# Performance work log

Measured on AMD Instinct MI355X. Metric: run time of the kernel, lower is better.

The kernel has to match this reference:

```python
import jax, jax.numpy as jnp
import numpy as np

HIDDEN = 256


def setup_inputs() -> dict:
    key = jax.random.key(0)
    ks = jax.random.split(key, 6)
    b, c_len, q_len, h = 32, 1024, 128, HIDDEN
    # Xavier-uniform bounds for the learned weights
    lim_vec = float(np.sqrt(6.0 / (h + 1)))      # (h, 1) weights
    lim_cq = float(np.sqrt(6.0 / (1 + h)))       # (1, 1, h) weight
    return {
        "context": jax.random.normal(ks[0], (b, c_len, h), dtype=jnp.float32),
        "query": jax.random.normal(ks[1], (b, q_len, h), dtype=jnp.float32),
        "c_mask": jnp.zeros((b, c_len), dtype=bool),
        "q_mask": jnp.zeros((b, q_len), dtype=bool),
        "c_weight": jax.random.uniform(ks[2], (h, 1), jnp.float32, -lim_vec, lim_vec),
        "q_weight": jax.random.uniform(ks[3], (h, 1), jnp.float32, -lim_vec, lim_vec),
        "cq_weight": jax.random.uniform(ks[4], (1, 1, h), jnp.float32, -lim_cq, lim_cq),
        "bias": jnp.zeros((1,), dtype=jnp.float32),
    }


def reference(context, query, c_mask, q_mask, c_weight, q_weight, cq_weight, bias):
    # Trilinear similarity: S[b,i,j] = c_i.w_c + q_j.w_q + (c_i * w_cq).q_j + bias
    s0 = context @ c_weight                                  # (b, c, 1)
    s1 = jnp.swapaxes(query @ q_weight, 1, 2)                # (b, 1, q)
    s2 = jnp.einsum('bch,bqh->bcq', context * cq_weight, query)
    S = s0 + s1 + s2 + bias                                  # (b, c, q)

    S_bar = jax.nn.softmax(S, axis=1)       # softmax over context axis
    S_bar_bar = jax.nn.softmax(S, axis=2)   # softmax over query axis

    A = jnp.einsum('bcq,bqh->bch', S, query)  # note: raw S, as in source
    B = jnp.einsum('bcq,bkq,bkh->bch', S_bar, S_bar_bar, context)

    return jnp.concatenate([context, A, context * A, context * B], axis=2)
```

## Files before the change

### kernel.cpp

```cpp
#include <hip/hip_runtime.h>
#include <cstdint>
#include <cstddef>

#define BATCH 32
#define CLEN  1024
#define QLEN  128
#define HID   256

typedef __attribute__((ext_vector_type(8))) short bf16x8;
typedef __attribute__((ext_vector_type(4))) float f32x4;

#define MFMA(a, b, c) __builtin_amdgcn_mfma_f32_16x16x32_bf16((a), (b), (c), 0, 0, 0)

__device__ __forceinline__ ushort f2b(float f) {
    union { float f; uint u; } v; v.f = f;
    uint r = (v.u + 0x7fffu + ((v.u >> 16) & 1u)) >> 16;
    return (ushort)r;
}
__device__ __forceinline__ float b2f(ushort u) {
    union { uint u; float f; } v; v.u = ((uint)u) << 16;
    return v.f;
}

__global__ __launch_bounds__(256) void prep_kernel(
    const float* __restrict__ context, const float* __restrict__ query,
    const float* __restrict__ cw, const float* __restrict__ qw,
    const float* __restrict__ cqw,
    ushort* __restrict__ ctxB, ushort* __restrict__ ctxT,
    ushort* __restrict__ qmB, ushort* __restrict__ qT,
    float* __restrict__ cdot, float* __restrict__ qdot)
{
    __shared__ ushort lds[64][258];
    int bid = blockIdx.x;
    int t = threadIdx.x;
    int r = t >> 2, qd = t & 3;
    if (bid < 512) {
        int b = bid >> 4, c0 = (bid & 15) * 64;
        const float* src = context + ((size_t)(b * CLEN + c0 + r)) * HID;
        ushort* cbr = ctxB + ((size_t)(b * CLEN + c0 + r)) * HID;
        float dot = 0.f;
        #pragma unroll
        for (int j = 0; j < 16; j++) {
            int h = j * 16 + qd * 4;
            float4 v = *reinterpret_cast<const float4*>(src + h);
            float4 w = *reinterpret_cast<const float4*>(cw + h);
            dot += v.x * w.x + v.y * w.y + v.z * w.z + v.w * w.w;
            uint p0 = (uint)f2b(v.x) | ((uint)f2b(v.y) << 16);
            uint p1 = (uint)f2b(v.z) | ((uint)f2b(v.w) << 16);
            *reinterpret_cast<uint*>(&lds[r][h])     = p0;
            *reinterpret_cast<uint*>(&lds[r][h + 2]) = p1;
            uint2 pk; pk.x = p0; pk.y = p1;
            *reinterpret_cast<uint2*>(cbr + h) = pk;
        }
        dot += __shfl_xor(dot, 1);
        dot += __shfl_xor(dot, 2);
        if (qd == 0) cdot[b * CLEN + c0 + r] = dot;
        __syncthreads();
        ushort* dst = ctxT + ((size_t)(b * HID + t)) * CLEN + c0;
        #pragma unroll
        for (int j = 0; j < 8; j++) {
            uint4 w;
            w.x = (uint)lds[j*8+0][t] | ((uint)lds[j*8+1][t] << 16);
            w.y = (uint)lds[j*8+2][t] | ((uint)lds[j*8+3][t] << 16);
            w.z = (uint)lds[j*8+4][t] | ((uint)lds[j*8+5][t] << 16);
            w.w = (uint)lds[j*8+6][t] | ((uint)lds[j*8+7][t] << 16);
            *reinterpret_cast<uint4*>(dst + j * 8) = w;
        }
    } else {
        int bb = bid - 512;
        int b = bb >> 1, q0 = (bb & 1) * 64;
        const float* src = query + ((size_t)(b * QLEN + q0 + r)) * HID;
        ushort* qmr = qmB + ((size_t)(b * QLEN + q0 + r)) * HID;
        float dot = 0.f;
        #pragma unroll
        for (int j = 0; j < 16; j++) {
            int h = j * 16 + qd * 4;
            float4 v   = *reinterpret_cast<const float4*>(src + h);
            float4 w   = *reinterpret_cast<const float4*>(qw + h);
            float4 wc4 = *reinterpret_cast<const float4*>(cqw + h);
            dot += v.x * w.x + v.y * w.y + v.z * w.z + v.w * w.w;
            uint p0 = (uint)f2b(v.x) | ((uint)f2b(v.y) << 16);
            uint p1 = (uint)f2b(v.z) | ((uint)f2b(v.w) << 16);
            *reinterpret_cast<uint*>(&lds[r][h])     = p0;
            *reinterpret_cast<uint*>(&lds[r][h + 2]) = p1;
            uint2 mc;
            mc.x = (uint)f2b(v.x * wc4.x) | ((uint)f2b(v.y * wc4.y) << 16);
            mc.y = (uint)f2b(v.z * wc4.z) | ((uint)f2b(v.w * wc4.w) << 16);
            *reinterpret_cast<uint2*>(qmr + h) = mc;
        }
        dot += __shfl_xor(dot, 1);
        dot += __shfl_xor(dot, 2);
        if (qd == 0) qdot[b * QLEN + q0 + r] = dot;
        __syncthreads();
        ushort* dst = qT + ((size_t)(b * HID + t)) * QLEN + q0;
        #pragma unroll
        for (int j = 0; j < 8; j++) {
            uint4 w;
            w.x = (uint)lds[j*8+0][t] | ((uint)lds[j*8+1][t] << 16);
            w.y = (uint)lds[j*8+2][t] | ((uint)lds[j*8+3][t] << 16);
            w.z = (uint)lds[j*8+4][t] | ((uint)lds[j*8+5][t] << 16);
            w.w = (uint)lds[j*8+6][t] | ((uint)lds[j*8+7][t] << 16);
            *reinterpret_cast<uint4*>(dst + j * 8) = w;
        }
    }
}

__global__ __launch_bounds__(256) void s_kernel(
    const ushort* __restrict__ ctxB, const ushort* __restrict__ qmB,
    const float* __restrict__ cdot, const float* __restrict__ qdot,
    const float* __restrict__ bias,
    ushort* __restrict__ S, ushort* __restrict__ P2T)
{
    __shared__ float ldsS[64][132];
    __shared__ float ldsM[64], ldsR[64];
    int ct = blockIdx.x, b = blockIdx.y;
    int c0 = ct * 64;
    int t = threadIdx.x;
    int w = t >> 6, L = t & 63, g = L >> 4, ln = L & 15;
    int wr = w >> 1, wc = w & 1;

    f32x4 acc[2][4];
    #pragma unroll
    for (int mi = 0; mi < 2; mi++)
        #pragma unroll
        for (int ni = 0; ni < 4; ni++) acc[mi][ni] = (f32x4){0.f, 0.f, 0.f, 0.f};

    const ushort* aBase = ctxB + ((size_t)(b * CLEN + c0 + wr * 32)) * HID;
    const ushort* qBb   = qmB + ((size_t)(b * QLEN + wc * 64)) * HID;

    #pragma unroll 2
    for (int kk = 0; kk < 8; kk++) {
        int k = kk * 32 + g * 8;
        bf16x8 a[2], bq[4];
        #pragma unroll
        for (int mi = 0; mi < 2; mi++)
            a[mi] = *reinterpret_cast<const bf16x8*>(aBase + (size_t)(mi * 16 + ln) * HID + k);
        #pragma unroll
        for (int ni = 0; ni < 4; ni++)
            bq[ni] = *reinterpret_cast<const bf16x8*>(qBb + (size_t)(ni * 16 + ln) * HID + k);
        #pragma unroll
        for (int mi = 0; mi < 2; mi++)
            #pragma unroll
            for (int ni = 0; ni < 4; ni++)
                acc[mi][ni] = MFMA(a[mi], bq[ni], acc[mi][ni]);
    }

    float bv = bias[0];
    float qdv[4];
    #pragma unroll
    for (int ni = 0; ni < 4; ni++) qdv[ni] = qdot[b * QLEN + wc * 64 + ni * 16 + ln];
    #pragma unroll
    for (int mi = 0; mi < 2; mi++)
        #pragma unroll
        for (int r = 0; r < 4; r++) {
            int row = wr * 32 + mi * 16 + g * 4 + r;
            float cd = cdot[b * CLEN + c0 + row] + bv;
            #pragma unroll
            for (int ni = 0; ni < 4; ni++)
                ldsS[row][wc * 64 + ni * 16 + ln] = acc[mi][ni][r] + cd + qdv[ni];
        }
    __syncthreads();
    {
        int row = t >> 2, qs = (t & 3) * 32;
        float4 vr[8];
        float m = -1e30f;
        #pragma unroll
        for (int j = 0; j < 8; j++) {
            vr[j] = *reinterpret_cast<const float4*>(&ldsS[row][qs + j * 4]);
            m = fmaxf(m, fmaxf(fmaxf(vr[j].x, vr[j].y), fmaxf(vr[j].z, vr[j].w)));
        }
        m = fmaxf(m, __shfl_xor(m, 1));
        m = fmaxf(m, __shfl_xor(m, 2));
        float s = 0.f;
        #pragma unroll
        for (int j = 0; j < 8; j++)
            s += __expf(vr[j].x - m) + __expf(vr[j].y - m) +
                 __expf(vr[j].z - m) + __expf(vr[j].w - m);
        s += __shfl_xor(s, 1);
        s += __shfl_xor(s, 2);
        if ((t & 3) == 0) { ldsM[row] = m; ldsR[row] = 1.0f / s; }
    }
    __syncthreads();
    {
        const size_t Sbase = ((size_t)b * CLEN + c0) * QLEN;
        #pragma unroll
        for (int i = 0; i < 8; i++) {
            int flat = t + 256 * i;
            int q4 = flat & 31, c = flat >> 5;
            float4 v = *reinterpret_cast<const float4*>(&ldsS[c][q4 * 4]);
            uint2 pk;
            pk.x = (uint)f2b(v.x) | ((uint)f2b(v.y) << 16);
            pk.y = (uint)f2b(v.z) | ((uint)f2b(v.w) << 16);
            *reinterpret_cast<uint2*>(&S[Sbase + (size_t)c * QLEN + q4 * 4]) = pk;
        }
    }
    {
        int q = t >> 1, half = t & 1;
        ushort* dst = P2T + ((size_t)b * QLEN + q) * CLEN + c0 + half * 32;
        #pragma unroll
        for (int jo = 0; jo < 4; jo++) {
            uint pk[4];
            #pragma unroll
            for (int l = 0; l < 4; l++) {
                int c0l = half * 32 + jo * 8 + l * 2;
                float p0 = __expf(ldsS[c0l][q]     - ldsM[c0l])     * ldsR[c0l];
                float p1 = __expf(ldsS[c0l + 1][q] - ldsM[c0l + 1]) * ldsR[c0l + 1];
                pk[l] = (uint)f2b(p0) | ((uint)f2b(p1) << 16);
            }
            uint4 wv; wv.x = pk[0]; wv.y = pk[1]; wv.z = pk[2]; wv.w = pk[3];
            *reinterpret_cast<uint4*>(dst + jo * 8) = wv;
        }
    }
}

__global__ __launch_bounds__(256) void t_kernel(
    const ushort* __restrict__ ctxT, const ushort* __restrict__ P2T,
    float* __restrict__ Tpart)
{
    int x = blockIdx.x, b = blockIdx.y;
    int h0 = (x >> 1) * 64, ks = x & 1;
    int t = threadIdx.x;
    int w = t >> 6, L = t & 63, g = L >> 4, ln = L & 15;
    int wr = w >> 1, wc = w & 1;

    f32x4 acc[2][4];
    #pragma unroll
    for (int mi = 0; mi < 2; mi++)
        #pragma unroll
        for (int ni = 0; ni < 4; ni++) acc[mi][ni] = (f32x4){0.f, 0.f, 0.f, 0.f};

    const ushort* aB = ctxT + ((size_t)(b * HID + h0 + wr * 32)) * CLEN + ks * 512;
    const ushort* bB = P2T + ((size_t)(b * QLEN + wc * 64)) * CLEN + ks * 512;

    #pragma unroll 2
    for (int kk = 0; kk < 16; kk++) {
        int k = kk * 32 + g * 8;
        bf16x8 a[2], bq[4];
        #pragma unroll
        for (int mi = 0; mi < 2; mi++)
            a[mi] = *reinterpret_cast<const bf16x8*>(aB + (size_t)(mi * 16 + ln) * CLEN + k);
        #pragma unroll
        for (int ni = 0; ni < 4; ni++)
            bq[ni] = *reinterpret_cast<const bf16x8*>(bB + (size_t)(ni * 16 + ln) * CLEN + k);
        #pragma unroll
        for (int mi = 0; mi < 2; mi++)
            #pragma unroll
            for (int ni = 0; ni < 4; ni++)
                acc[mi][ni] = MFMA(a[mi], bq[ni], acc[mi][ni]);
    }
    float* dst = Tpart + (size_t)ks * (BATCH * HID * QLEN);
    #pragma unroll
    for (int mi = 0; mi < 2; mi++)
        #pragma unroll
        for (int ni = 0; ni < 4; ni++)
            #pragma unroll
            for (int r = 0; r < 4; r++) {
                int h = h0 + wr * 32 + mi * 16 + g * 4 + r;
                int q = wc * 64 + ni * 16 + ln;
                dst[((size_t)b * HID + h) * QLEN + q] = acc[mi][ni][r];
            }
}

__global__ __launch_bounds__(256) void cs_kernel(
    const ushort* __restrict__ S, const float* __restrict__ Tpart,
    ushort* __restrict__ Tt)
{
    __shared__ float red[4][2][8];
    __shared__ float SR[16];
    int qc = blockIdx.x, b = blockIdx.y;
    int q0 = qc * 16;
    int t = threadIdx.x;
    int qh = t & 1, cg = t >> 1;
    int w = t >> 6, L = t & 63;
    const ushort* base = S + (size_t)b * CLEN * QLEN + q0 + qh * 8;
    float sum[8];
    #pragma unroll
    for (int j = 0; j < 8; j++) sum[j] = 0.f;
    #pragma unroll
    for (int i = 0; i < 8; i++) {
        bf16x8 v = *reinterpret_cast<const bf16x8*>(base + (size_t)(cg + 128 * i) * QLEN);
        #pragma unroll
        for (int j = 0; j < 8; j++) sum[j] += __expf(b2f((ushort)v[j]));
    }
    #pragma unroll
    for (int off = 2; off <= 32; off <<= 1)
        #pragma unroll
        for (int j = 0; j < 8; j++) sum[j] += __shfl_xor(sum[j], off, 64);
    if (L < 2) {
        #pragma unroll
        for (int j = 0; j < 8; j++) red[w][L][j] = sum[j];
    }
    __syncthreads();
    if (t < 16) {
        int j = t & 7, qq = t >> 3;
        float s = red[0][qq][j] + red[1][qq][j] + red[2][qq][j] + red[3][qq][j];
        SR[qq * 8 + j] = 1.0f / s;
    }
    __syncthreads();
    const float* p0 = Tpart + ((size_t)b * HID + t) * QLEN + q0;
    const float* p1 = p0 + (size_t)BATCH * HID * QLEN;
    uint pk[8];
    #pragma unroll
    for (int seg = 0; seg < 4; seg++) {
        float4 xa = *reinterpret_cast<const float4*>(p0 + seg * 4);
        float4 xb = *reinterpret_cast<const float4*>(p1 + seg * 4);
        float r0 = (xa.x + xb.x) * SR[seg * 4 + 0];
        float r1 = (xa.y + xb.y) * SR[seg * 4 + 1];
        float r2 = (xa.z + xb.z) * SR[seg * 4 + 2];
        float r3 = (xa.w + xb.w) * SR[seg * 4 + 3];
        pk[seg * 2 + 0] = (uint)f2b(r0) | ((uint)f2b(r1) << 16);
        pk[seg * 2 + 1] = (uint)f2b(r2) | ((uint)f2b(r3) << 16);
    }
    ushort* dst = Tt + ((size_t)b * HID + t) * QLEN + q0;
    uint4 w0; w0.x = pk[0]; w0.y = pk[1]; w0.z = pk[2]; w0.w = pk[3];
    uint4 w1; w1.x = pk[4]; w1.y = pk[5]; w1.z = pk[6]; w1.w = pk[7];
    *reinterpret_cast<uint4*>(dst)     = w0;
    *reinterpret_cast<uint4*>(dst + 8) = w1;
}

__global__ __launch_bounds__(256) void ab_out_kernel(
    const ushort* __restrict__ S, const ushort* __restrict__ qT,
    const ushort* __restrict__ Tt, const ushort* __restrict__ ctxB,
    float* __restrict__ out)
{
    __shared__ float ldsA[64][68];
    __shared__ float ldsB[64][68];
    int x = blockIdx.x, b = blockIdx.y;
    int c0 = (x >> 1) * 64, h0 = (x & 1) * 128;
    int t = threadIdx.x;
    int wv = t >> 6, L = t & 63, g = L >> 4, ln = L & 15;

    f32x4 accA[4][2], accB[4][2];
    #pragma unroll
    for (int mi = 0; mi < 4; mi++)
        #pragma unroll
        for (int ni = 0; ni < 2; ni++) {
            accA[mi][ni] = (f32x4){0.f, 0.f, 0.f, 0.f};
            accB[mi][ni] = (f32x4){0.f, 0.f, 0.f, 0.f};
        }

    const ushort* Srow = S + ((size_t)(b * CLEN + c0)) * QLEN;
    const ushort* qTb  = qT + ((size_t)(b * HID + h0 + wv * 32)) * QLEN;
    const ushort* TtB  = Tt + ((size_t)(b * HID + h0 + wv * 32)) * QLEN;

    #pragma unroll
    for (int kk = 0; kk < 4; kk++) {
        int k = kk * 32 + g * 8;
        bf16x8 sa[4], pa[4], bq[2], bt[2];
        #pragma unroll
        for (int mi = 0; mi < 4; mi++) {
            sa[mi] = *reinterpret_cast<const bf16x8*>(Srow + (size_t)(mi * 16 + ln) * QLEN + k);
            bf16x8 pv;
            #pragma unroll
            for (int i = 0; i < 8; i++)
                pv[i] = (short)f2b(__expf(b2f((ushort)sa[mi][i])));
            pa[mi] = pv;
        }
        #pragma unroll
        for (int ni = 0; ni < 2; ni++) {
            bq[ni] = *reinterpret_cast<const bf16x8*>(qTb + (size_t)(ni * 16 + ln) * QLEN + k);
            bt[ni] = *reinterpret_cast<const bf16x8*>(TtB + (size_t)(ni * 16 + ln) * QLEN + k);
        }
        #pragma unroll
        for (int mi = 0; mi < 4; mi++)
            #pragma unroll
            for (int ni = 0; ni < 2; ni++) {
                accA[mi][ni] = MFMA(sa[mi], bq[ni], accA[mi][ni]);
                accB[mi][ni] = MFMA(pa[mi], bt[ni], accB[mi][ni]);
            }
    }

    #pragma unroll
    for (int hh = 0; hh < 2; hh++) {
        if ((wv >> 1) == hh) {
            int hc = wv & 1;
            #pragma unroll
            for (int mi = 0; mi < 4; mi++)
                #pragma unroll
                for (int ni = 0; ni < 2; ni++)
                    #pragma unroll
                    for (int r = 0; r < 4; r++) {
                        ldsA[mi * 16 + g * 4 + r][hc * 32 + ni * 16 + ln] = accA[mi][ni][r];
                        ldsB[mi * 16 + g * 4 + r][hc * 32 + ni * 16 + ln] = accB[mi][ni][r];
                    }
        }
        __syncthreads();
        #pragma unroll
        for (int i = 0; i < 2; i++) {
            int flat = t + 256 * i;
            int h8 = flat & 7, c = flat >> 3;
            bf16x8 cb = *reinterpret_cast<const bf16x8*>(
                ctxB + ((size_t)(b * CLEN + c0 + c)) * HID + h0 + hh * 64 + h8 * 8);
            float cf[8];
            #pragma unroll
            for (int j = 0; j < 8; j++) cf[j] = b2f((ushort)cb[j]);
            float4 a0 = *reinterpret_cast<const float4*>(&ldsA[c][h8 * 8]);
            float4 a1 = *reinterpret_cast<const float4*>(&ldsA[c][h8 * 8 + 4]);
            float4 b0 = *reinterpret_cast<const float4*>(&ldsB[c][h8 * 8]);
            float4 b1 = *reinterpret_cast<const float4*>(&ldsB[c][h8 * 8 + 4]);
            size_t o = ((size_t)(b * CLEN + c0 + c)) * 1024 + h0 + hh * 64 + h8 * 8;
            *reinterpret_cast<float4*>(&out[o])     = make_float4(cf[0], cf[1], cf[2], cf[3]);
            *reinterpret_cast<float4*>(&out[o + 4]) = make_float4(cf[4], cf[5], cf[6], cf[7]);
            *reinterpret_cast<float4*>(&out[o + 256]) = a0;
            *reinterpret_cast<float4*>(&out[o + 260]) = a1;
            *reinterpret_cast<float4*>(&out[o + 512]) =
                make_float4(cf[0] * a0.x, cf[1] * a0.y, cf[2] * a0.z, cf[3] * a0.w);
            *reinterpret_cast<float4*>(&out[o + 516]) =
                make_float4(cf[4] * a1.x, cf[5] * a1.y, cf[6] * a1.z, cf[7] * a1.w);
            *reinterpret_cast<float4*>(&out[o + 768]) =
                make_float4(cf[0] * b0.x, cf[1] * b0.y, cf[2] * b0.z, cf[3] * b0.w);
            *reinterpret_cast<float4*>(&out[o + 772]) =
                make_float4(cf[4] * b1.x, cf[5] * b1.y, cf[6] * b1.z, cf[7] * b1.w);
        }
        __syncthreads();
    }
}

extern "C" void kernel_launch(void* const* d_in, const int* in_sizes, int n_in,
                              void* d_out, int out_size, void* d_ws, size_t ws_size,
                              hipStream_t stream)
{
    (void)in_sizes; (void)n_in; (void)out_size; (void)ws_size;
    const float* context   = (const float*)d_in[0];
    const float* query     = (const float*)d_in[1];
    const float* c_weight  = (const float*)d_in[4];
    const float* q_weight  = (const float*)d_in[5];
    const float* cq_weight = (const float*)d_in[6];
    const float* bias      = (const float*)d_in[7];
    float* out = (float*)d_out;
    char* wsb  = (char*)d_ws;

    ushort* ctxB = (ushort*)(wsb);
    ushort* ctxT = (ushort*)(wsb + 16777216);
    ushort* qmB  = (ushort*)(wsb + 33554432);
    ushort* qT   = (ushort*)(wsb + 35651584);
    ushort* S    = (ushort*)(wsb + 37748736);
    ushort* P2T  = (ushort*)(wsb + 46137344);
    ushort* Tt   = (ushort*)(wsb + 54525952);
    float*  Tpart = (float*)(wsb + 56623104);
    float*  cdot  = (float*)(wsb + 65011712);
    float*  qdot  = cdot + 32768;

    prep_kernel<<<576, 256, 0, stream>>>(context, query, c_weight, q_weight,
                                         cq_weight, ctxB, ctxT, qmB, qT,
                                         cdot, qdot);
    s_kernel<<<dim3(16, 32), 256, 0, stream>>>(ctxB, qmB, cdot, qdot, bias, S, P2T);
    t_kernel<<<dim3(8, 32), 256, 0, stream>>>(ctxT, P2T, Tpart);
    cs_kernel<<<dim3(8, 32), 256, 0, stream>>>(S, Tpart, Tt);
    ab_out_kernel<<<dim3(32, 32), 256, 0, stream>>>(S, qT, Tt, ctxB, out);
}
```

Before: 105.9 us.

## Fuse column-softmax sums into S kernel and restructure T and output stages

The S kernel now also emits per-tile column sums of exp(S), so the separate column-sum pass over S in cs_kernel goes away. The reciprocal column sum is applied to P when forming the B operand in ab_out, and cs_kernel becomes a simple elementwise reduce-and-convert kernel. t_kernel's split-K goes from 2 to 4 to launch more blocks, which adds Tpart traffic. Block indices in several kernels are remapped so that blocks sharing a batch run together, likely for L2 locality. The ab_out tile changes to 32 rows by the full hidden width.

Result: slower. 122.9 us (+16.1%).

```diff
diff --git a/kernel.cpp b/kernel.cpp
--- a/kernel.cpp
+++ b/kernel.cpp
@@ -109,11 +109,16 @@
     const ushort* __restrict__ ctxB, const ushort* __restrict__ qmB,
     const float* __restrict__ cdot, const float* __restrict__ qdot,
     const float* __restrict__ bias,
-    ushort* __restrict__ S, ushort* __restrict__ P2T)
+    ushort* __restrict__ S, ushort* __restrict__ P2T,
+    float* __restrict__ psum)
 {
     __shared__ float ldsS[64][132];
     __shared__ float ldsM[64], ldsR[64];
-    int ct = blockIdx.x, b = blockIdx.y;
+    __shared__ float ldsP[2][128];
+    int lin = blockIdx.x + (blockIdx.y << 4);
+    int m = lin >> 3;
+    int b = (lin & 7) | ((m >> 4) << 3);
+    int ct = m & 15;
     int c0 = ct * 64;
     int t = threadIdx.x;
     int w = t >> 6, L = t & 63, g = L >> 4, ln = L & 15;
@@ -163,22 +168,22 @@
     {
         int row = t >> 2, qs = (t & 3) * 32;
         float4 vr[8];
-        float m = -1e30f;
+        float mx = -1e30f;
         #pragma unroll
         for (int j = 0; j < 8; j++) {
             vr[j] = *reinterpret_cast<const float4*>(&ldsS[row][qs + j * 4]);
-            m = fmaxf(m, fmaxf(fmaxf(vr[j].x, vr[j].y), fmaxf(vr[j].z, vr[j].w)));
-        }
-        m = fmaxf(m, __shfl_xor(m, 1));
-        m = fmaxf(m, __shfl_xor(m, 2));
+            mx = fmaxf(mx, fmaxf(fmaxf(vr[j].x, vr[j].y), fmaxf(vr[j].z, vr[j].w)));
+        }
+        mx = fmaxf(mx, __shfl_xor(mx, 1));
+        mx = fmaxf(mx, __shfl_xor(mx, 2));
         float s = 0.f;
         #pragma unroll
         for (int j = 0; j < 8; j++)
-            s += __expf(vr[j].x - m) + __expf(vr[j].y - m) +
-                 __expf(vr[j].z - m) + __expf(vr[j].w - m);
+            s += __expf(vr[j].x - mx) + __expf(vr[j].y - mx) +
+                 __expf(vr[j].z - mx) + __expf(vr[j].w - mx);
         s += __shfl_xor(s, 1);
         s += __shfl_xor(s, 2);
-        if ((t & 3) == 0) { ldsM[row] = m; ldsR[row] = 1.0f / s; }
+        if ((t & 3) == 0) { ldsM[row] = mx; ldsR[row] = 1.0f / s; }
     }
     __syncthreads();
     {
@@ -211,15 +216,37 @@
             *reinterpret_cast<uint4*>(dst + jo * 8) = wv;
         }
     }
+    {
+        int q = t & 127, hf = t >> 7;
+        float s = 0.f;
+        #pragma unroll
+        for (int cc = 0; cc < 32; cc++)
+            s += __expf(b2f(f2b(ldsS[hf * 32 + cc][q])));
+        ldsP[hf][q] = s;
+    }
+    __syncthreads();
+    if (t < 128)
+        psum[((size_t)b * 16 + ct) * QLEN + t] = ldsP[0][t] + ldsP[1][t];
 }
 
 __global__ __launch_bounds__(256) void t_kernel(
     const ushort* __restrict__ ctxT, const ushort* __restrict__ P2T,
-    float* __restrict__ Tpart)
-{
-    int x = blockIdx.x, b = blockIdx.y;
-    int h0 = (x >> 1) * 64, ks = x & 1;
+    const float* __restrict__ psum, float* __restrict__ Tpart,
+    float* __restrict__ colsumr)
+{
+    int lin = blockIdx.x + (blockIdx.y << 4);
+    int m = lin >> 3;
+    int b = (lin & 7) | ((m >> 4) << 3);
+    int x = m & 15;
+    int h0 = (x >> 2) * 64, ks = x & 3;
     int t = threadIdx.x;
+    if (x == 0 && t < QLEN) {
+        float s = 0.f;
+        #pragma unroll
+        for (int j = 0; j < 16; j++)
+            s += psum[((size_t)b * 16 + j) * QLEN + t];
+        colsumr[b * QLEN + t] = 1.0f / s;
+    }
     int w = t >> 6, L = t & 63, g = L >> 4, ln = L & 15;
     int wr = w >> 1, wc = w & 1;
 
@@ -229,11 +256,11 @@
         #pragma unroll
         for (int ni = 0; ni < 4; ni++) acc[mi][ni] = (f32x4){0.f, 0.f, 0.f, 0.f};
 
-    const ushort* aB = ctxT + ((size_t)(b * HID + h0 + wr * 32)) * CLEN + ks * 512;
-    const ushort* bB = P2T + ((size_t)(b * QLEN + wc * 64)) * CLEN + ks * 512;
+    const ushort* aB = ctxT + ((size_t)(b * HID + h0 + wr * 32)) * CLEN + ks * 256;
+    const ushort* bB = P2T + ((size_t)(b * QLEN + wc * 64)) * CLEN + ks * 256;
 
     #pragma unroll 2
-    for (int kk = 0; kk < 16; kk++) {
+    for (int kk = 0; kk < 8; kk++) {
         int k = kk * 32 + g * 8;
         bf16x8 a[2], bq[4];
         #pragma unroll
@@ -261,156 +288,125 @@
             }
 }
 
-__global__ __launch_bounds__(256) void cs_kernel(
-    const ushort* __restrict__ S, const float* __restrict__ Tpart,
-    ushort* __restrict__ Tt)
-{
-    __shared__ float red[4][2][8];
-    __shared__ float SR[16];
-    int qc = blockIdx.x, b = blockIdx.y;
-    int q0 = qc * 16;
-    int t = threadIdx.x;
-    int qh = t & 1, cg = t >> 1;
-    int w = t >> 6, L = t & 63;
-    const ushort* base = S + (size_t)b * CLEN * QLEN + q0 + qh * 8;
-    float sum[8];
-    #pragma unroll
-    for (int j = 0; j < 8; j++) sum[j] = 0.f;
-    #pragma unroll
-    for (int i = 0; i < 8; i++) {
-        bf16x8 v = *reinterpret_cast<const bf16x8*>(base + (size_t)(cg + 128 * i) * QLEN);
-        #pragma unroll
-        for (int j = 0; j < 8; j++) sum[j] += __expf(b2f((ushort)v[j]));
-    }
-    #pragma unroll
-    for (int off = 2; off <= 32; off <<= 1)
-        #pragma unroll
-        for (int j = 0; j < 8; j++) sum[j] += __shfl_xor(sum[j], off, 64);
-    if (L < 2) {
-        #pragma unroll
-        for (int j = 0; j < 8; j++) red[w][L][j] = sum[j];
-    }
-    __syncthreads();
-    if (t < 16) {
-        int j = t & 7, qq = t >> 3;
-        float s = red[0][qq][j] + red[1][qq][j] + red[2][qq][j] + red[3][qq][j];
-        SR[qq * 8 + j] = 1.0f / s;
-    }
-    __syncthreads();
-    const float* p0 = Tpart + ((size_t)b * HID + t) * QLEN + q0;
-    const float* p1 = p0 + (size_t)BATCH * HID * QLEN;
-    uint pk[8];
-    #pragma unroll
-    for (int seg = 0; seg < 4; seg++) {
-        float4 xa = *reinterpret_cast<const float4*>(p0 + seg * 4);
-        float4 xb = *reinterpret_cast<const float4*>(p1 + seg * 4);
-        float r0 = (xa.x + xb.x) * SR[seg * 4 + 0];
-        float r1 = (xa.y + xb.y) * SR[seg * 4 + 1];
-        float r2 = (xa.z + xb.z) * SR[seg * 4 + 2];
-        float r3 = (xa.w + xb.w) * SR[seg * 4 + 3];
-        pk[seg * 2 + 0] = (uint)f2b(r0) | ((uint)f2b(r1) << 16);
-        pk[seg * 2 + 1] = (uint)f2b(r2) | ((uint)f2b(r3) << 16);
-    }
-    ushort* dst = Tt + ((size_t)b * HID + t) * QLEN + q0;
-    uint4 w0; w0.x = pk[0]; w0.y = pk[1]; w0.z = pk[2]; w0.w = pk[3];
-    uint4 w1; w1.x = pk[4]; w1.y = pk[5]; w1.z = pk[6]; w1.w = pk[7];
-    *reinterpret_cast<uint4*>(dst)     = w0;
-    *reinterpret_cast<uint4*>(dst + 8) = w1;
+__global__ __launch_bounds__(256) void tr_kernel(
+    const float* __restrict__ Tpart, ushort* __restrict__ Tt)
+{
+    int gid = blockIdx.x * 256 + threadIdx.x;
+    const float4* p = reinterpret_cast<const float4*>(Tpart);
+    float4 a = p[gid];
+    float4 b = p[gid + 262144];
+    float4 c = p[gid + 524288];
+    float4 d = p[gid + 786432];
+    float4 r = make_float4(a.x + b.x + c.x + d.x, a.y + b.y + c.y + d.y,
+                           a.z + b.z + c.z + d.z, a.w + b.w + c.w + d.w);
+    uint2 pk;
+    pk.x = (uint)f2b(r.x) | ((uint)f2b(r.y) << 16);
+    pk.y = (uint)f2b(r.z) | ((uint)f2b(r.w) << 16);
+    *reinterpret_cast<uint2*>(Tt + (size_t)gid * 4) = pk;
 }
 
 __global__ __launch_bounds__(256) void ab_out_kernel(
     const ushort* __restrict__ S, const ushort* __restrict__ qT,
     const ushort* __restrict__ Tt, const ushort* __restrict__ ctxB,
-    float* __restrict__ out)
-{
-    __shared__ float ldsA[64][68];
-    __shared__ float ldsB[64][68];
-    int x = blockIdx.x, b = blockIdx.y;
-    int c0 = (x >> 1) * 64, h0 = (x & 1) * 128;
+    const float* __restrict__ colsumr, float* __restrict__ out)
+{
+    __shared__ float ldsA[16][260];
+    __shared__ float ldsB[16][260];
+    int lin = blockIdx.x + (blockIdx.y << 5);
+    int m = lin >> 3;
+    int b = (lin & 7) | ((m >> 5) << 3);
+    int ct = m & 31;
+    int c0 = ct * 32;
     int t = threadIdx.x;
     int wv = t >> 6, L = t & 63, g = L >> 4, ln = L & 15;
-
-    f32x4 accA[4][2], accB[4][2];
-    #pragma unroll
-    for (int mi = 0; mi < 4; mi++)
-        #pragma unroll
-        for (int ni = 0; ni < 2; ni++) {
+    int h0w = wv * 64;
+
+    f32x4 accA[2][4], accB[2][4];
+    #pragma unroll
+    for (int mi = 0; mi < 2; mi++)
+        #pragma unroll
+        for (int ni = 0; ni < 4; ni++) {
             accA[mi][ni] = (f32x4){0.f, 0.f, 0.f, 0.f};
             accB[mi][ni] = (f32x4){0.f, 0.f, 0.f, 0.f};
         }
 
     const ushort* Srow = S + ((size_t)(b * CLEN + c0)) * QLEN;
-    const ushort* qTb  = qT + ((size_t)(b * HID + h0 + wv * 32)) * QLEN;
-    const ushort* TtB  = Tt + ((size_t)(b * HID + h0 + wv * 32)) * QLEN;
+    const ushort* qTb  = qT + ((size_t)(b * HID + h0w)) * QLEN;
+    const ushort* TtB  = Tt + ((size_t)(b * HID + h0w)) * QLEN;
+    const float* crB = colsumr + b * QLEN;
 
     #pragma unroll
     for (int kk = 0; kk < 4; kk++) {
         int k = kk * 32 + g * 8;
-        bf16x8 sa[4], pa[4], bq[2], bt[2];
-        #pragma unroll
-        for (int mi = 0; mi < 4; mi++) {
+        float4 cr0 = *reinterpret_cast<const float4*>(crB + k);
+        float4 cr1 = *reinterpret_cast<const float4*>(crB + k + 4);
+        float crv[8] = {cr0.x, cr0.y, cr0.z, cr0.w, cr1.x, cr1.y, cr1.z, cr1.w};
+        bf16x8 sa[2], pa[2], bq[4], bt[4];
+        #pragma unroll
+        for (int mi = 0; mi < 2; mi++) {
             sa[mi] = *reinterpret_cast<const bf16x8*>(Srow + (size_t)(mi * 16 + ln) * QLEN + k);
             bf16x8 pv;
             #pragma unroll
             for (int i = 0; i < 8; i++)
-                pv[i] = (short)f2b(__expf(b2f((ushort)sa[mi][i])));
+                pv[i] = (short)f2b(__expf(b2f((ushort)sa[mi][i])) * crv[i]);
             pa[mi] = pv;
         }
         #pragma unroll
-        for (int ni = 0; ni < 2; ni++) {
+        for (int ni = 0; ni < 4; ni++) {
             bq[ni] = *reinterpret_cast<const bf16x8*>(qTb + (size_t)(ni * 16 + ln) * QLEN + k);
             bt[ni] = *reinterpret_cast<const bf16x8*>(TtB + (size_t)(ni * 16 + ln) * QLEN + k);
         }
         #pragma unroll
-        for (int mi = 0; mi < 4; mi++)
-            #pragma unroll
-            for (int ni = 0; ni < 2; ni++) {
+        for (int mi = 0; mi < 2; mi++)
+            #pragma unroll
+            for (int ni = 0; ni < 4; ni++) {
                 accA[mi][ni] = MFMA(sa[mi], bq[ni], accA[mi][ni]);
                 accB[mi][ni] = MFMA(pa[mi], bt[ni], accB[mi][ni]);
             }
     }
 
     #pragma unroll
-    for (int hh = 0; hh < 2; hh++) {
-        if ((wv >> 1) == hh) {
-            int hc = wv & 1;
-            #pragma unroll
-            for (int mi = 0; mi < 4; mi++)
-                #pragma unroll
-                for (int ni = 0; ni < 2; ni++)
-                    #pragma unroll
-                    for (int r = 0; r < 4; r++) {
-                        ldsA[mi * 16 + g * 4 + r][hc * 32 + ni * 16 + ln] = accA[mi][ni][r];
-                        ldsB[mi * 16 + g * 4 + r][hc * 32 + ni * 16 + ln] = accB[mi][ni][r];
-                    }
-        }
+    for (int ch = 0; ch < 2; ch++) {
+        #pragma unroll
+        for (int ni = 0; ni < 4; ni++)
+            #pragma unroll
+            for (int r = 0; r < 4; r++) {
+                ldsA[g * 4 + r][h0w + ni * 16 + ln] = accA[ch][ni][r];
+                ldsB[g * 4 + r][h0w + ni * 16 + ln] = accB[ch][ni][r];
+            }
         __syncthreads();
-        #pragma unroll
-        for (int i = 0; i < 2; i++) {
-            int flat = t + 256 * i;
-            int h8 = flat & 7, c = flat >> 3;
-            bf16x8 cb = *reinterpret_cast<const bf16x8*>(
-                ctxB + ((size_t)(b * CLEN + c0 + c)) * HID + h0 + hh * 64 + h8 * 8);
-            float cf[8];
-            #pragma unroll
-            for (int j = 0; j < 8; j++) cf[j] = b2f((ushort)cb[j]);
-            float4 a0 = *reinterpret_cast<const float4*>(&ldsA[c][h8 * 8]);
-            float4 a1 = *reinterpret_cast<const float4*>(&ldsA[c][h8 * 8 + 4]);
-            float4 b0 = *reinterpret_cast<const float4*>(&ldsB[c][h8 * 8]);
-            float4 b1 = *reinterpret_cast<const float4*>(&ldsB[c][h8 * 8 + 4]);
-            size_t o = ((size_t)(b * CLEN + c0 + c)) * 1024 + h0 + hh * 64 + h8 * 8;
-            *reinterpret_cast<float4*>(&out[o])     = make_float4(cf[0], cf[1], cf[2], cf[3]);
-            *reinterpret_cast<float4*>(&out[o + 4]) = make_float4(cf[4], cf[5], cf[6], cf[7]);
-            *reinterpret_cast<float4*>(&out[o + 256]) = a0;
-            *reinterpret_cast<float4*>(&out[o + 260]) = a1;
-            *reinterpret_cast<float4*>(&out[o + 512]) =
-                make_float4(cf[0] * a0.x, cf[1] * a0.y, cf[2] * a0.z, cf[3] * a0.w);
-            *reinterpret_cast<float4*>(&out[o + 516]) =
-                make_float4(cf[4] * a1.x, cf[5] * a1.y, cf[6] * a1.z, cf[7] * a1.w);
-            *reinterpret_cast<float4*>(&out[o + 768]) =
-                make_float4(cf[0] * b0.x, cf[1] * b0.y, cf[2] * b0.z, cf[3] * b0.w);
-            *reinterpret_cast<float4*>(&out[o + 772]) =
-                make_float4(cf[4] * b1.x, cf[5] * b1.y, cf[6] * b1.z, cf[7] * b1.w);
+        {
+            int cl = t >> 4, hseg = t & 15;
+            int c = c0 + ch * 16 + cl;
+            const ushort* cbp = ctxB + ((size_t)(b * CLEN + c)) * HID + hseg * 16;
+            bf16x8 cb0 = *reinterpret_cast<const bf16x8*>(cbp);
+            bf16x8 cb1 = *reinterpret_cast<const bf16x8*>(cbp + 8);
+            float cf[16];
+            #pragma unroll
+            for (int j = 0; j < 8; j++) {
+                cf[j]     = b2f((ushort)cb0[j]);
+                cf[j + 8] = b2f((ushort)cb1[j]);
+            }
+            float av[16], bv[16];
+            #pragma unroll
+            for (int j = 0; j < 16; j += 4) {
+                float4 a4 = *reinterpret_cast<const float4*>(&ldsA[cl][hseg * 16 + j]);
+                float4 b4 = *reinterpret_cast<const float4*>(&ldsB[cl][hseg * 16 + j]);
+                av[j] = a4.x; av[j+1] = a4.y; av[j+2] = a4.z; av[j+3] = a4.w;
+                bv[j] = b4.x; bv[j+1] = b4.y; bv[j+2] = b4.z; bv[j+3] = b4.w;
+            }
+            size_t o = ((size_t)(b * CLEN + c)) * 1024 + hseg * 16;
+            #pragma unroll
+            for (int j = 0; j < 16; j += 4) {
+                *reinterpret_cast<float4*>(&out[o + j]) =
+                    make_float4(cf[j], cf[j+1], cf[j+2], cf[j+3]);
+                *reinterpret_cast<float4*>(&out[o + 256 + j]) =
+                    make_float4(av[j], av[j+1], av[j+2], av[j+3]);
+                *reinterpret_cast<float4*>(&out[o + 512 + j]) =
+                    make_float4(cf[j]*av[j], cf[j+1]*av[j+1], cf[j+2]*av[j+2], cf[j+3]*av[j+3]);
+                *reinterpret_cast<float4*>(&out[o + 768 + j]) =
+                    make_float4(cf[j]*bv[j], cf[j+1]*bv[j+1], cf[j+2]*bv[j+2], cf[j+3]*bv[j+3]);
+            }
         }
         __syncthreads();
     }
@@ -438,14 +434,17 @@
     ushort* P2T  = (ushort*)(wsb + 46137344);
     ushort* Tt   = (ushort*)(wsb + 54525952);
     float*  Tpart = (float*)(wsb + 56623104);
-    float*  cdot  = (float*)(wsb + 65011712);
-    float*  qdot  = cdot + 32768;
+    float*  cdot    = (float*)(wsb + 73400320);
+    float*  qdot    = cdot + 32768;
+    float*  colsumr = qdot + 4096;
+    float*  psum    = colsumr + 4096;
 
     prep_kernel<<<576, 256, 0, stream>>>(context, query, c_weight, q_weight,
                                          cq_weight, ctxB, ctxT, qmB, qT,
                                          cdot, qdot);
-    s_kernel<<<dim3(16, 32), 256, 0, stream>>>(ctxB, qmB, cdot, qdot, bias, S, P2T);
-    t_kernel<<<dim3(8, 32), 256, 0, stream>>>(ctxT, P2T, Tpart);
-    cs_kernel<<<dim3(8, 32), 256, 0, stream>>>(S, Tpart, Tt);
-    ab_out_kernel<<<dim3(32, 32), 256, 0, stream>>>(S, qT, Tt, ctxB, out);
-}
+    s_kernel<<<dim3(16, 32), 256, 0, stream>>>(ctxB, qmB, cdot, qdot, bias,
+                                               S, P2T, psum);
+    t_kernel<<<dim3(16, 32), 256, 0, stream>>>(ctxT, P2T, psum, Tpart, colsumr);
+    tr_kernel<<<1024, 256, 0, stream>>>(Tpart, Tt);
+    ab_out_kernel<<<dim3(32, 32), 256, 0, stream>>>(S, qT, Tt, ctxB, colsumr, out);
+}
```

## Fuse column softmax partial sums into S kernel, drop S re-read in cs_kernel

Applied to the files above, without the earlier changes.

The S kernel now computes per-tile column exp-sums (using bf16-rounded S values to match the prior path) and writes them to a small psum buffer. cs_kernel then reduces 16 partials per query instead of re-reading the whole 8 MB bf16 S matrix, and is re-tiled over hidden rows. The ab_out block index mapping also changes so consecutive blocks share h0 and walk c. The cost is extra exp work and one more barrier in the S kernel.

Measured after the change: 99.82 us, median of 2. -5.7%, faster.

```diff
diff --git a/kernel.cpp b/kernel.cpp
--- a/kernel.cpp
+++ b/kernel.cpp
@@ -109,10 +109,12 @@
     const ushort* __restrict__ ctxB, const ushort* __restrict__ qmB,
     const float* __restrict__ cdot, const float* __restrict__ qdot,
     const float* __restrict__ bias,
-    ushort* __restrict__ S, ushort* __restrict__ P2T)
+    ushort* __restrict__ S, ushort* __restrict__ P2T,
+    float* __restrict__ psum)
 {
     __shared__ float ldsS[64][132];
     __shared__ float ldsM[64], ldsR[64];
+    __shared__ float ldsP[2][128];
     int ct = blockIdx.x, b = blockIdx.y;
     int c0 = ct * 64;
     int t = threadIdx.x;
@@ -163,22 +165,22 @@
     {
         int row = t >> 2, qs = (t & 3) * 32;
         float4 vr[8];
-        float m = -1e30f;
+        float mx = -1e30f;
         #pragma unroll
         for (int j = 0; j < 8; j++) {
             vr[j] = *reinterpret_cast<const float4*>(&ldsS[row][qs + j * 4]);
-            m = fmaxf(m, fmaxf(fmaxf(vr[j].x, vr[j].y), fmaxf(vr[j].z, vr[j].w)));
-        }
-        m = fmaxf(m, __shfl_xor(m, 1));
-        m = fmaxf(m, __shfl_xor(m, 2));
+            mx = fmaxf(mx, fmaxf(fmaxf(vr[j].x, vr[j].y), fmaxf(vr[j].z, vr[j].w)));
+        }
+        mx = fmaxf(mx, __shfl_xor(mx, 1));
+        mx = fmaxf(mx, __shfl_xor(mx, 2));
         float s = 0.f;
         #pragma unroll
         for (int j = 0; j < 8; j++)
-            s += __expf(vr[j].x - m) + __expf(vr[j].y - m) +
-                 __expf(vr[j].z - m) + __expf(vr[j].w - m);
+            s += __expf(vr[j].x - mx) + __expf(vr[j].y - mx) +
+                 __expf(vr[j].z - mx) + __expf(vr[j].w - mx);
         s += __shfl_xor(s, 1);
         s += __shfl_xor(s, 2);
-        if ((t & 3) == 0) { ldsM[row] = m; ldsR[row] = 1.0f / s; }
+        if ((t & 3) == 0) { ldsM[row] = mx; ldsR[row] = 1.0f / s; }
     }
     __syncthreads();
     {
@@ -211,6 +213,17 @@
             *reinterpret_cast<uint4*>(dst + jo * 8) = wv;
         }
     }
+    {
+        int q = t & 127, hf = t >> 7;
+        float s = 0.f;
+        #pragma unroll
+        for (int cc = 0; cc < 32; cc++)
+            s += __expf(b2f(f2b(ldsS[hf * 32 + cc][q])));
+        ldsP[hf][q] = s;
+    }
+    __syncthreads();
+    if (t < 128)
+        psum[((size_t)b * 16 + ct) * QLEN + t] = ldsP[0][t] + ldsP[1][t];
 }
 
 __global__ __launch_bounds__(256) void t_kernel(
@@ -262,56 +275,36 @@
 }
 
 __global__ __launch_bounds__(256) void cs_kernel(
-    const ushort* __restrict__ S, const float* __restrict__ Tpart,
+    const float* __restrict__ psum, const float* __restrict__ Tpart,
     ushort* __restrict__ Tt)
 {
-    __shared__ float red[4][2][8];
-    __shared__ float SR[16];
-    int qc = blockIdx.x, b = blockIdx.y;
-    int q0 = qc * 16;
+    __shared__ float SR[128];
+    int hc = blockIdx.x, b = blockIdx.y;
     int t = threadIdx.x;
-    int qh = t & 1, cg = t >> 1;
-    int w = t >> 6, L = t & 63;
-    const ushort* base = S + (size_t)b * CLEN * QLEN + q0 + qh * 8;
-    float sum[8];
-    #pragma unroll
-    for (int j = 0; j < 8; j++) sum[j] = 0.f;
-    #pragma unroll
-    for (int i = 0; i < 8; i++) {
-        bf16x8 v = *reinterpret_cast<const bf16x8*>(base + (size_t)(cg + 128 * i) * QLEN);
-        #pragma unroll
-        for (int j = 0; j < 8; j++) sum[j] += __expf(b2f((ushort)v[j]));
-    }
-    #pragma unroll
-    for (int off = 2; off <= 32; off <<= 1)
-        #pragma unroll
-        for (int j = 0; j < 8; j++) sum[j] += __shfl_xor(sum[j], off, 64);
-    if (L < 2) {
-        #pragma unroll
-        for (int j = 0; j < 8; j++) red[w][L][j] = sum[j];
+    if (t < 128) {
+        float s = 0.f;
+        #pragma unroll
+        for (int j = 0; j < 16; j++)
+            s += psum[((size_t)b * 16 + j) * QLEN + t];
+        SR[t] = 1.0f / s;
     }
     __syncthreads();
-    if (t < 16) {
-        int j = t & 7, qq = t >> 3;
-        float s = red[0][qq][j] + red[1][qq][j] + red[2][qq][j] + red[3][qq][j];
-        SR[qq * 8 + j] = 1.0f / s;
-    }
-    __syncthreads();
-    const float* p0 = Tpart + ((size_t)b * HID + t) * QLEN + q0;
+    int h = hc * 32 + (t >> 3), qs = (t & 7) * 16;
+    const float* p0 = Tpart + ((size_t)b * HID + h) * QLEN + qs;
     const float* p1 = p0 + (size_t)BATCH * HID * QLEN;
     uint pk[8];
     #pragma unroll
     for (int seg = 0; seg < 4; seg++) {
         float4 xa = *reinterpret_cast<const float4*>(p0 + seg * 4);
         float4 xb = *reinterpret_cast<const float4*>(p1 + seg * 4);
-        float r0 = (xa.x + xb.x) * SR[seg * 4 + 0];
-        float r1 = (xa.y + xb.y) * SR[seg * 4 + 1];
-        float r2 = (xa.z + xb.z) * SR[seg * 4 + 2];
-        float r3 = (xa.w + xb.w) * SR[seg * 4 + 3];
+        float r0 = (xa.x + xb.x) * SR[qs + seg * 4 + 0];
+        float r1 = (xa.y + xb.y) * SR[qs + seg * 4 + 1];
+        float r2 = (xa.z + xb.z) * SR[qs + seg * 4 + 2];
+        float r3 = (xa.w + xb.w) * SR[qs + seg * 4 + 3];
         pk[seg * 2 + 0] = (uint)f2b(r0) | ((uint)f2b(r1) << 16);
         pk[seg * 2 + 1] = (uint)f2b(r2) | ((uint)f2b(r3) << 16);
     }
-    ushort* dst = Tt + ((size_t)b * HID + t) * QLEN + q0;
+    ushort* dst = Tt + ((size_t)b * HID + h) * QLEN + qs;
     uint4 w0; w0.x = pk[0]; w0.y = pk[1]; w0.z = pk[2]; w0.w = pk[3];
     uint4 w1; w1.x = pk[4]; w1.y = pk[5]; w1.z = pk[6]; w1.w = pk[7];
     *reinterpret_cast<uint4*>(dst)     = w0;
@@ -326,7 +319,7 @@
     __shared__ float ldsA[64][68];
     __shared__ float ldsB[64][68];
     int x = blockIdx.x, b = blockIdx.y;
-    int c0 = (x >> 1) * 64, h0 = (x & 1) * 128;
+    int c0 = (x & 15) * 64, h0 = (x >> 4) * 128;
     int t = threadIdx.x;
     int wv = t >> 6, L = t & 63, g = L >> 4, ln = L & 15;
 
@@ -440,12 +433,14 @@
     float*  Tpart = (float*)(wsb + 56623104);
     float*  cdot  = (float*)(wsb + 65011712);
     float*  qdot  = cdot + 32768;
+    float*  psum  = qdot + 4096;
 
     prep_kernel<<<576, 256, 0, stream>>>(context, query, c_weight, q_weight,
                                          cq_weight, ctxB, ctxT, qmB, qT,
                                          cdot, qdot);
-    s_kernel<<<dim3(16, 32), 256, 0, stream>>>(ctxB, qmB, cdot, qdot, bias, S, P2T);
+    s_kernel<<<dim3(16, 32), 256, 0, stream>>>(ctxB, qmB, cdot, qdot, bias,
+                                               S, P2T, psum);
     t_kernel<<<dim3(8, 32), 256, 0, stream>>>(ctxT, P2T, Tpart);
-    cs_kernel<<<dim3(8, 32), 256, 0, stream>>>(S, Tpart, Tt);
+    cs_kernel<<<dim3(8, 32), 256, 0, stream>>>(psum, Tpart, Tt);
     ab_out_kernel<<<dim3(32, 32), 256, 0, stream>>>(S, qT, Tt, ctxB, out);
 }
```
